# Performance work log

Hardware: AMD Instinct MI355X
Metric: run time of the kernel (lower is better)

## Reference

```python
import jax, jax.numpy as jnp
import numpy as np

B, T, F = 2048, 2048, 16
WINDOW = 24


def _pool_mat(L, S):
    # PyTorch AdaptiveAvgPool1d: bin i averages indices [floor(i*L/S), ceil((i+1)*L/S))
    M = np.zeros((S, L), np.float32)
    for i in range(S):
        s = (i * L) // S
        e = -((-(i + 1) * L) // S)
        M[i, s:e] = 1.0 / (e - s)
    return jnp.asarray(M)


def _conv1d(x, w, dil):
    # x: [B, Cin, L], w: [Cout, Cin, K], VALID, rhs-dilated
    return jax.lax.conv_general_dilated(
        x, w, window_strides=(1,), padding='VALID', rhs_dilation=(dil,),
        dimension_numbers=('NCH', 'OIH', 'NCH'))


def _forward(x, was, wbs, wfc):
    xc = jnp.transpose(x, (0, 2, 1))  # [B, F, T]
    t = x.shape[1]
    feats = []
    for k in range(1, 7):
        # stage a: conv(F->1, kernel k, dil 1) -> adaptive pool to 12 -> leaky relu
        fa = _conv1d(xc, was[k - 1], 1)  # [B, 1, t-k+1]
        fa = jax.nn.leaky_relu(
            jnp.einsum('bcl,sl->bcs', fa, _pool_mat(t - (k - 1), WINDOW // 2)), 0.1)
        # stage b: conv(1->1, kernel k, dil 2) on fa -> adaptive pool to 6 -> leaky relu
        lb = WINDOW // 2 - 2 * (k - 1)  # 12, 10, 8, 6, 4, 2
        fb = _conv1d(fa, wbs[k - 1], 2)  # [B, 1, lb]
        fb = jax.nn.leaky_relu(
            jnp.einsum('bcl,sl->bcs', fb, _pool_mat(lb, WINDOW // 4)), 0.1)
        feats += [fa, fb]  # cat order: f1a, f1b, f2a, f2b, ...
    h = jnp.concatenate(feats, axis=2).reshape(x.shape[0], -1)  # [B, 108]
    return h @ wfc.T  # [B, 1]


def setup_inputs() -> dict:
    key = jax.random.key(0)
    ks = jax.random.split(key, 14)
    inp = {'x': jax.random.normal(ks[0], (B, T, F), jnp.float32)}
    for k in range(1, 7):
        inp[f'wa{k}'] = jax.random.normal(ks[k], (1, F, k), jnp.float32) * 0.1
        inp[f'wb{k}'] = jax.random.normal(ks[6 + k], (1, 1, k), jnp.float32) * 0.3
    inp['wfc'] = jax.random.normal(ks[13], (1, 108), jnp.float32) * 0.1
    return inp


def reference(x, wa1, wa2, wa3, wa4, wa5, wa6,
              wb1, wb2, wb3, wb4, wb5, wb6, wfc):
    was = [wa1, wa2, wa3, wa4, wa5, wa6]
    wbs = [wb1, wb2, wb3, wb4, wb5, wb6]
    return _forward(x, was, wbs, wfc)
```

## Files before the change

### kernel.cpp

```cpp
#include <hip/hip_runtime.h>

#define NCH 16
#define TLEN 2048
#define NTHREADS 256
#define PAD 20

__global__ __launch_bounds__(NTHREADS, 4) void filternet_kernel(
    const float* __restrict__ x,
    const float* __restrict__ wa1, const float* __restrict__ wa2,
    const float* __restrict__ wa3, const float* __restrict__ wa4,
    const float* __restrict__ wa5, const float* __restrict__ wa6,
    const float* __restrict__ wb1, const float* __restrict__ wb2,
    const float* __restrict__ wb3, const float* __restrict__ wb4,
    const float* __restrict__ wb5, const float* __restrict__ wb6,
    const float* __restrict__ wfc, float* __restrict__ out, int nb)
{
    __shared__ float xWin[13 * 16][PAD];
    __shared__ float sWinBase[13][16];
    __shared__ float blkSum[4][16];
    __shared__ float waL[6][NCH][6];
    __shared__ float wbL[6][6];
    __shared__ float wfcL[108];
    __shared__ float faL[6][12];
    __shared__ float partial[6];

    const int tid = threadIdx.x;
    const int b = blockIdx.x;
    if (b >= nb) return;
    const float* __restrict__ xb = x + (size_t)b * (TLEN * NCH);

    const int l  = tid & 63;
    const int w  = tid >> 6;
    const int g  = l & 3;

    float4 wv0, wv1, wv2, wv3;
    if (tid < 13 * 16) {
        const int ci = tid >> 4, off = tid & 15;
        const int cb = (ci == 0) ? 0 : (ci * 2043) / 12 - 1;
        const int p = cb + off;
        if (p < TLEN) {
            const float4* xr = reinterpret_cast<const float4*>(xb) + (size_t)p * 4;
            wv0 = xr[0]; wv1 = xr[1]; wv2 = xr[2]; wv3 = xr[3];
        } else {
            wv0 = wv1 = wv2 = wv3 = make_float4(0.f, 0.f, 0.f, 0.f);
        }
    }

    if (tid < 96) {
        const int k0 = tid >> 4, c = tid & 15, K = k0 + 1;
        const float* wp = (k0 == 0) ? wa1 : (k0 == 1) ? wa2 : (k0 == 2) ? wa3
                        : (k0 == 3) ? wa4 : (k0 == 4) ? wa5 : wa6;
        for (int j = 0; j < 6; ++j)
            waL[k0][c][j] = (j < K) ? wp[c * K + j] : 0.0f;
    } else if (tid < 102) {
        const int k0 = tid - 96, K = k0 + 1;
        const float* wp = (k0 == 0) ? wb1 : (k0 == 1) ? wb2 : (k0 == 2) ? wb3
                        : (k0 == 3) ? wb4 : (k0 == 4) ? wb5 : wb6;
        for (int j = 0; j < 6; ++j)
            wbL[k0][j] = (j < K) ? wp[j] : 0.0f;
    } else if (tid >= 128 && tid < 236) {
        wfcL[tid - 128] = wfc[tid - 128];
    }

    int qv0, qv1, qv2, qv3;
    {
        int qt[4];
#pragma unroll
        for (int s = 0; s < 4; ++s) {
            const int ci = 3 * w + s;
            const int cb = (ci == 0) ? 0 : (ci * 2043) / 12 - 1;
            const int r  = cb - (w << 9);
            qt[s] = (r >= 0 && r <= 512) ? ((r + 15) >> 4) : -1;
        }
        qv0 = __builtin_amdgcn_readfirstlane(qt[0]);
        qv1 = __builtin_amdgcn_readfirstlane(qt[1]);
        qv2 = __builtin_amdgcn_readfirstlane(qt[2]);
        qv3 = __builtin_amdgcn_readfirstlane(qt[3]);
    }

    float4 acc = make_float4(0.f, 0.f, 0.f, 0.f);
    float4 sn0 = acc, sn1 = acc, sn2 = acc, sn3 = acc;
    const float4* x4 = reinterpret_cast<const float4*>(xb) + ((size_t)w * 2048 + l);
#pragma unroll 4
    for (int it = 0; it < 32; ++it) {
        if (it == qv0) sn0 = acc;
        if (it == qv1) sn1 = acc;
        if (it == qv2) sn2 = acc;
        if (it == qv3) sn3 = acc;
        float4 v = x4[64 * it];
        acc.x += v.x; acc.y += v.y; acc.z += v.z; acc.w += v.w;
    }
    if (qv0 == 32) sn0 = acc;
    if (qv1 == 32) sn1 = acc;
    if (qv2 == 32) sn2 = acc;
    if (qv3 == 32) sn3 = acc;

    {
        float4 t = acc;
#pragma unroll
        for (int m = 4; m <= 32; m <<= 1) {
            t.x += __shfl_xor(t.x, m, 64); t.y += __shfl_xor(t.y, m, 64);
            t.z += __shfl_xor(t.z, m, 64); t.w += __shfl_xor(t.w, m, 64);
        }
        if (l < 4) *reinterpret_cast<float4*>(&blkSum[w][l * 4]) = t;
    }
#pragma unroll
    for (int s = 0; s < 4; ++s) {
        const int q = (s == 0) ? qv0 : (s == 1) ? qv1 : (s == 2) ? qv2 : qv3;
        if (q >= 0) {
            float4 t = (s == 0) ? sn0 : (s == 1) ? sn1 : (s == 2) ? sn2 : sn3;
#pragma unroll
            for (int m = 4; m <= 32; m <<= 1) {
                t.x += __shfl_xor(t.x, m, 64); t.y += __shfl_xor(t.y, m, 64);
                t.z += __shfl_xor(t.z, m, 64); t.w += __shfl_xor(t.w, m, 64);
            }
            if (l < 4) *reinterpret_cast<float4*>(&sWinBase[3 * w + s][l * 4]) = t;
        }
    }

    if (tid < 13 * 16) {
        float4* dst = reinterpret_cast<float4*>(&xWin[tid][0]);
        dst[0] = wv0; dst[1] = wv1; dst[2] = wv2; dst[3] = wv3;
    }
    __syncthreads();

    if (tid < 13 * 16) {
        const int ci = tid >> 4, c = tid & 15;
        const int cb = (ci == 0) ? 0 : (ci * 2043) / 12 - 1;
        const int wb = cb >> 9;
        const int r  = cb - (wb << 9);
        const int qc = (r + 15) >> 4;
        const int ov = (qc << 4) - r;
        float run = sWinBase[ci][c];
        for (int wp = 0; wp < wb; ++wp) run += blkSum[wp][c];
        for (int o = 0; o < ov; ++o) run -= xWin[ci * 16 + o][c];
#pragma unroll
        for (int off = 0; off < 16; ++off) {
            const int p = cb + off;
            const float v = xWin[ci * 16 + off][c];
            xWin[ci * 16 + off][c] = run;
            if (p < TLEN) run += v;
        }
    }
    __syncthreads();

    if (tid < 72) {
        const int k0 = tid / 12, i = tid % 12, K = k0 + 1;
        const int L = TLEN - k0;
        const int s = (i * L) / 12;
        const int e = ((i + 1) * L + 11) / 12;
        const int n = e - s;
        const int cbs = (i == 0) ? 0 : (i * 2043) / 12 - 1;
        const int cbe = ((i + 1) * 2043) / 12 - 1;
        const int rs = i * 16 + (s - cbs);
        const int re = (i + 1) * 16 + (e - cbe);
        float acc2 = 0.0f;
        for (int j = 0; j < K; ++j) {
#pragma unroll
            for (int c = 0; c < NCH; ++c)
                acc2 += waL[k0][c][j] * (xWin[re + j][c] - xWin[rs + j][c]);
        }
        float v = acc2 / (float)n;
        faL[k0][i] = (v >= 0.0f) ? v : 0.1f * v;
    }
    __syncthreads();

    if (tid < 6) {
        const int k0 = tid, K = k0 + 1;
        const int lb = 12 - 2 * k0;
        float fbv[12];
        for (int lo = 0; lo < lb; ++lo) {
            float a = 0.0f;
            for (int j = 0; j < K; ++j) a += wbL[k0][j] * faL[k0][lo + 2 * j];
            fbv[lo] = a;
        }
        float part = 0.0f;
        for (int i2 = 0; i2 < 12; ++i2)
            part += faL[k0][i2] * wfcL[k0 * 18 + i2];
        for (int i6 = 0; i6 < 6; ++i6) {
            const int s6 = (i6 * lb) / 6;
            const int e6 = ((i6 + 1) * lb + 5) / 6;
            float v = 0.0f;
            for (int lo = s6; lo < e6; ++lo) v += fbv[lo];
            v /= (float)(e6 - s6);
            v = (v >= 0.0f) ? v : 0.1f * v;
            part += v * wfcL[k0 * 18 + 12 + i6];
        }
        partial[k0] = part;
    }
    __syncthreads();

    if (tid == 0) {
        out[b] = partial[0] + partial[1] + partial[2] +
                 partial[3] + partial[4] + partial[5];
    }
}

extern "C" void kernel_launch(void* const* d_in, const int* in_sizes, int n_in,
                              void* d_out, int out_size, void* d_ws, size_t ws_size,
                              hipStream_t stream) {
    const float* x = nullptr;
    const float* wa[6] = {nullptr};
    const float* wb[6] = {nullptr};
    const float* wfc = nullptr;
    int nb = 0;
    for (int i = 0; i < n_in; ++i) {
        const int sz = in_sizes[i];
        const float* p = (const float*)d_in[i];
        if (sz >= TLEN * NCH) { x = p; nb = sz / (TLEN * NCH); }
        else if (sz == 108)   { wfc = p; }
        else if (sz % NCH == 0 && sz >= NCH && sz <= 6 * NCH) { wa[sz / NCH - 1] = p; }
        else if (sz >= 1 && sz <= 6) { wb[sz - 1] = p; }
    }

    float* outp = (float*)d_out;
    dim3 grid(nb), block(NTHREADS);
    hipLaunchKernelGGL(filternet_kernel, grid, block, 0, stream,
                       x, wa[0], wa[1], wa[2], wa[3], wa[4], wa[5],
                       wb[0], wb[1], wb[2], wb[3], wb[4], wb[5],
                       wfc, outp, nb);
}
```

Baseline: 71.84 us.

## Split fused kernel into streaming prefix-sum kernel and tail kernel via workspace

Splits the single kernel into two launches. The first streams x and writes per-wave block sums and window-boundary prefix snapshots to global workspace. The second reloads those values plus the window rows and does the conv, pool and FC tail. The aim is a lean, high-occupancy streaming kernel separated from the shared-memory-heavy tail. It costs an extra launch, a workspace round trip and re-reading about 208 rows of x per sample.

```diff
diff --git a/kernel.cpp b/kernel.cpp
--- a/kernel.cpp
+++ b/kernel.cpp
@@ -5,8 +5,82 @@
 #define NTHREADS 256
 #define PAD 20
 
-__global__ __launch_bounds__(NTHREADS, 4) void filternet_kernel(
-    const float* __restrict__ x,
+__global__ __launch_bounds__(NTHREADS) void filternet_stream(
+    const float* __restrict__ x, float* __restrict__ ws, int nb)
+{
+    const int tid = threadIdx.x;
+    const int b = blockIdx.x;
+    if (b >= nb) return;
+    const float* __restrict__ xb = x + (size_t)b * (TLEN * NCH);
+
+    const int l = tid & 63;
+    const int w = tid >> 6;
+
+    int qv0, qv1, qv2, qv3;
+    {
+        int qt[4];
+#pragma unroll
+        for (int s = 0; s < 4; ++s) {
+            const int ci = 3 * w + s;
+            const int cb = (ci == 0) ? 0 : (ci * 2043) / 12 - 1;
+            const int r  = cb - (w << 9);
+            qt[s] = (r >= 0 && r <= 512) ? ((r + 15) >> 4) : -1;
+        }
+        qv0 = __builtin_amdgcn_readfirstlane(qt[0]);
+        qv1 = __builtin_amdgcn_readfirstlane(qt[1]);
+        qv2 = __builtin_amdgcn_readfirstlane(qt[2]);
+        qv3 = __builtin_amdgcn_readfirstlane(qt[3]);
+    }
+
+    float4 acc = make_float4(0.f, 0.f, 0.f, 0.f);
+    float4 sn0 = acc, sn1 = acc, sn2 = acc, sn3 = acc;
+    const float4* x4 = reinterpret_cast<const float4*>(xb) + ((size_t)w * 2048 + l);
+#pragma unroll 4
+    for (int it = 0; it < 32; ++it) {
+        if (it == qv0) sn0 = acc;
+        if (it == qv1) sn1 = acc;
+        if (it == qv2) sn2 = acc;
+        if (it == qv3) sn3 = acc;
+        float4 v = x4[64 * it];
+        acc.x += v.x; acc.y += v.y; acc.z += v.z; acc.w += v.w;
+    }
+    if (qv0 == 32) sn0 = acc;
+    if (qv1 == 32) sn1 = acc;
+    if (qv2 == 32) sn2 = acc;
+    if (qv3 == 32) sn3 = acc;
+
+    float* wsBlk = ws;
+    float* wsWin = ws + (size_t)nb * 64;
+
+    {
+        float4 t = acc;
+#pragma unroll
+        for (int m = 4; m <= 32; m <<= 1) {
+            t.x += __shfl_xor(t.x, m, 64); t.y += __shfl_xor(t.y, m, 64);
+            t.z += __shfl_xor(t.z, m, 64); t.w += __shfl_xor(t.w, m, 64);
+        }
+        if (l < 4)
+            *reinterpret_cast<float4*>(wsBlk + (size_t)b * 64 + w * 16 + l * 4) = t;
+    }
+#pragma unroll
+    for (int s = 0; s < 4; ++s) {
+        const int q = (s == 0) ? qv0 : (s == 1) ? qv1 : (s == 2) ? qv2 : qv3;
+        if (q >= 0) {
+            float4 t = (s == 0) ? sn0 : (s == 1) ? sn1 : (s == 2) ? sn2 : sn3;
+#pragma unroll
+            for (int m = 4; m <= 32; m <<= 1) {
+                t.x += __shfl_xor(t.x, m, 64); t.y += __shfl_xor(t.y, m, 64);
+                t.z += __shfl_xor(t.z, m, 64); t.w += __shfl_xor(t.w, m, 64);
+            }
+            if (l < 4)
+                *reinterpret_cast<float4*>(
+                    wsWin + (size_t)b * 208 + (3 * w + s) * 16 + l * 4) = t;
+        }
+    }
+}
+
+__global__ __launch_bounds__(NTHREADS, 4) void filternet_tail(
+    const float* __restrict__ x, const float* __restrict__ ws,
     const float* __restrict__ wa1, const float* __restrict__ wa2,
     const float* __restrict__ wa3, const float* __restrict__ wa4,
     const float* __restrict__ wa5, const float* __restrict__ wa6,
@@ -16,8 +90,8 @@
     const float* __restrict__ wfc, float* __restrict__ out, int nb)
 {
     __shared__ float xWin[13 * 16][PAD];
-    __shared__ float sWinBase[13][16];
-    __shared__ float blkSum[4][16];
+    __shared__ float sWinBaseL[13][16];
+    __shared__ float blkSumL[4][16];
     __shared__ float waL[6][NCH][6];
     __shared__ float wbL[6][6];
     __shared__ float wfcL[108];
@@ -28,10 +102,8 @@
     const int b = blockIdx.x;
     if (b >= nb) return;
     const float* __restrict__ xb = x + (size_t)b * (TLEN * NCH);
-
-    const int l  = tid & 63;
-    const int w  = tid >> 6;
-    const int g  = l & 3;
+    const float* wsBlk = ws;
+    const float* wsWin = ws + (size_t)nb * 64;
 
     float4 wv0, wv1, wv2, wv3;
     if (tid < 13 * 16) {
@@ -43,6 +115,19 @@
             wv0 = xr[0]; wv1 = xr[1]; wv2 = xr[2]; wv3 = xr[3];
         } else {
             wv0 = wv1 = wv2 = wv3 = make_float4(0.f, 0.f, 0.f, 0.f);
+        }
+    }
+
+    if (tid >= 208) {
+        const int base = (tid - 208) * 6;
+        for (int u = 0; u < 6; ++u) {
+            const int i = base + u;
+            if (i < 272) {
+                const float v = (i < 64) ? wsBlk[(size_t)b * 64 + i]
+                                         : wsWin[(size_t)b * 208 + (i - 64)];
+                if (i < 64) ((float*)blkSumL)[i] = v;
+                else        ((float*)sWinBaseL)[i - 64] = v;
+            }
         }
     }
 
@@ -58,64 +143,10 @@
                         : (k0 == 3) ? wb4 : (k0 == 4) ? wb5 : wb6;
         for (int j = 0; j < 6; ++j)
             wbL[k0][j] = (j < K) ? wp[j] : 0.0f;
-    } else if (tid >= 128 && tid < 236) {
-        wfcL[tid - 128] = wfc[tid - 128];
-    }
-
-    int qv0, qv1, qv2, qv3;
-    {
-        int qt[4];
-#pragma unroll
-        for (int s = 0; s < 4; ++s) {
-            const int ci = 3 * w + s;
-            const int cb = (ci == 0) ? 0 : (ci * 2043) / 12 - 1;
-            const int r  = cb - (w << 9);
-            qt[s] = (r >= 0 && r <= 512) ? ((r + 15) >> 4) : -1;
-        }
-        qv0 = __builtin_amdgcn_readfirstlane(qt[0]);
-        qv1 = __builtin_amdgcn_readfirstlane(qt[1]);
-        qv2 = __builtin_amdgcn_readfirstlane(qt[2]);
-        qv3 = __builtin_amdgcn_readfirstlane(qt[3]);
-    }
-
-    float4 acc = make_float4(0.f, 0.f, 0.f, 0.f);
-    float4 sn0 = acc, sn1 = acc, sn2 = acc, sn3 = acc;
-    const float4* x4 = reinterpret_cast<const float4*>(xb) + ((size_t)w * 2048 + l);
-#pragma unroll 4
-    for (int it = 0; it < 32; ++it) {
-        if (it == qv0) sn0 = acc;
-        if (it == qv1) sn1 = acc;
-        if (it == qv2) sn2 = acc;
-        if (it == qv3) sn3 = acc;
-        float4 v = x4[64 * it];
-        acc.x += v.x; acc.y += v.y; acc.z += v.z; acc.w += v.w;
-    }
-    if (qv0 == 32) sn0 = acc;
-    if (qv1 == 32) sn1 = acc;
-    if (qv2 == 32) sn2 = acc;
-    if (qv3 == 32) sn3 = acc;
-
-    {
-        float4 t = acc;
-#pragma unroll
-        for (int m = 4; m <= 32; m <<= 1) {
-            t.x += __shfl_xor(t.x, m, 64); t.y += __shfl_xor(t.y, m, 64);
-            t.z += __shfl_xor(t.z, m, 64); t.w += __shfl_xor(t.w, m, 64);
-        }
-        if (l < 4) *reinterpret_cast<float4*>(&blkSum[w][l * 4]) = t;
-    }
-#pragma unroll
-    for (int s = 0; s < 4; ++s) {
-        const int q = (s == 0) ? qv0 : (s == 1) ? qv1 : (s == 2) ? qv2 : qv3;
-        if (q >= 0) {
-            float4 t = (s == 0) ? sn0 : (s == 1) ? sn1 : (s == 2) ? sn2 : sn3;
-#pragma unroll
-            for (int m = 4; m <= 32; m <<= 1) {
-                t.x += __shfl_xor(t.x, m, 64); t.y += __shfl_xor(t.y, m, 64);
-                t.z += __shfl_xor(t.z, m, 64); t.w += __shfl_xor(t.w, m, 64);
-            }
-            if (l < 4) *reinterpret_cast<float4*>(&sWinBase[3 * w + s][l * 4]) = t;
-        }
+    } else if (tid >= 128 && tid < 208) {
+        const int i0 = (tid - 128) * 2;
+        if (i0 < 108)     wfcL[i0] = wfc[i0];
+        if (i0 + 1 < 108) wfcL[i0 + 1] = wfc[i0 + 1];
     }
 
     if (tid < 13 * 16) {
@@ -131,8 +162,8 @@
         const int r  = cb - (wb << 9);
         const int qc = (r + 15) >> 4;
         const int ov = (qc << 4) - r;
-        float run = sWinBase[ci][c];
-        for (int wp = 0; wp < wb; ++wp) run += blkSum[wp][c];
+        float run = sWinBaseL[ci][c];
+        for (int wp = 0; wp < wb; ++wp) run += blkSumL[wp][c];
         for (int o = 0; o < ov; ++o) run -= xWin[ci * 16 + o][c];
 #pragma unroll
         for (int off = 0; off < 16; ++off) {
@@ -213,10 +244,12 @@
         else if (sz >= 1 && sz <= 6) { wb[sz - 1] = p; }
     }
 
+    float* wsf = (float*)d_ws;
     float* outp = (float*)d_out;
     dim3 grid(nb), block(NTHREADS);
-    hipLaunchKernelGGL(filternet_kernel, grid, block, 0, stream,
-                       x, wa[0], wa[1], wa[2], wa[3], wa[4], wa[5],
+    hipLaunchKernelGGL(filternet_stream, grid, block, 0, stream, x, wsf, nb);
+    hipLaunchKernelGGL(filternet_tail, grid, block, 0, stream,
+                       x, wsf, wa[0], wa[1], wa[2], wa[3], wa[4], wa[5],
                        wb[0], wb[1], wb[2], wb[3], wb[4], wb[5],
                        wfc, outp, nb);
 }
```

Result: slower. 79.41 us (+10.5%).
